# Kernel tuning notes

Measured on AMD Instinct MI355X. Metric: run time of the kernel, lower is better.

Reference implementation:

```python
import jax, jax.numpy as jnp
import numpy as np

# NTU RGB+D 25-joint skeleton edges (1-based)
NTU_EDGES = [(1,2),(2,21),(3,21),(4,3),(5,21),(6,5),(7,6),(8,7),(9,21),(10,9),
             (11,10),(12,11),(13,1),(14,13),(15,14),(16,15),(17,1),(18,17),
             (19,18),(20,19),(22,23),(23,8),(24,25),(25,12)]
NUM_SCALES = 13
NUM_POINT = 25


def build_A_powers(num_scales=NUM_SCALES, v=NUM_POINT):
    # MS-G3D disentangled multi-scale aggregation: exact-k-hop adjacencies, each
    # with self loops, symmetrically normalized, stacked along dim 0 -> (K*V, V).
    A = np.zeros((v, v))
    for i, j in NTU_EDGES:
        A[i - 1, j - 1] = 1.0
        A[j - 1, i - 1] = 1.0
    I = np.eye(v)
    mats = []
    for k in range(num_scales):
        if k == 0:
            Ak = I.copy()
        else:
            Ak = np.minimum(np.linalg.matrix_power(A + I, k), 1) \
               - np.minimum(np.linalg.matrix_power(A + I, k - 1), 1)
            Ak = Ak + I  # with_self=True
        d = Ak.sum(-1)
        dinv = np.where(d > 0, d ** -0.5, 0.0)
        mats.append((dinv[:, None] * Ak) * dinv[None, :])
    return np.concatenate(mats, 0).astype(np.float32)


def batchnorm(x, g, b, axes, ch_axis, eps=1e-5):
    # torch BatchNorm in training mode: biased batch stats + affine
    mean = jnp.mean(x, axes, keepdims=True)
    var = jnp.mean((x - mean) ** 2, axes, keepdims=True)
    shape = [1] * x.ndim
    shape[ch_axis] = -1
    return (x - mean) * jax.lax.rsqrt(var + eps) * g.reshape(shape) + b.reshape(shape)


def ms_gcn(x, A_powers, A_res, W, b, g, beta, num_scales):
    # x: (N, C, T, V); A: (K*V, V)
    A = A_powers + A_res
    support = jnp.einsum('vu,nctu->nctv', A, x)            # (N, C, T, K*V)
    N, C, T, KV = support.shape
    V = KV // num_scales
    support = support.reshape(N, C, T, num_scales, V).transpose(0, 3, 1, 2, 4)
    support = support.reshape(N, num_scales * C, T, V)     # (N, K*C, T, V)
    out = jnp.einsum('oc,nctv->notv', W, support) + b[None, :, None, None]  # 1x1 conv
    out = batchnorm(out, g, beta, (0, 2, 3), 1)
    return jax.nn.relu(out)


def lstm(x, Wih, Whh, bih, bhh):
    # single-layer batch_first LSTM, zero initial state; torch gate order i,f,g,o
    B = x.shape[0]
    H = Whh.shape[1]
    xp = jnp.einsum('bsd,hd->bsh', x, Wih) + bih + bhh     # precompute input proj

    def step(carry, xt):
        h, c = carry
        gates = xt + h @ Whh.T
        i, f, g, o = jnp.split(gates, 4, axis=-1)
        c = jax.nn.sigmoid(f) * c + jax.nn.sigmoid(i) * jnp.tanh(g)
        h = jax.nn.sigmoid(o) * jnp.tanh(c)
        return (h, c), h

    init = (jnp.zeros((B, H), x.dtype), jnp.zeros((B, H), x.dtype))
    _, ys = jax.lax.scan(step, init, jnp.swapaxes(xp, 0, 1))
    return jnp.swapaxes(ys, 0, 1)                          # (B, S, H)


def logsig_rnn(x, n_segments, Wih, Whh, bih, bhh):
    # x: (B, T, d). Depth-2 log-signature per time segment + segment start point,
    # concatenated and fed to an LSTM (Logsig-RNN layer).
    B, T, d = x.shape
    t_vec = np.array([int(round(float(v))) for v in np.linspace(1, T, n_segments + 1)])
    starts = t_vec[:-1] - 1
    ends = t_vec[1:] - 1
    L = int((ends - starts).max()) + 1
    # pad segments to fixed length by repeating the last point (zero increments)
    idx = np.minimum(starts[:, None] + np.arange(L)[None, :], ends[:, None])  # (S, L)
    pts = x[:, idx, :]                                     # (B, S, L, d)
    rel = pts - pts[:, :, :1, :]
    inc = rel[:, :, -1, :]                                 # level-1: total increment
    dx = pts[:, :, 1:, :] - pts[:, :, :-1, :]
    Mm = jnp.einsum('bsli,bslj->bsij', rel[:, :, :-1, :], dx)
    iu, ju = np.triu_indices(d, k=1)
    levy = 0.5 * (Mm[:, :, iu, ju] - Mm[:, :, ju, iu])     # level-2 (Lyndon basis)
    feats = jnp.concatenate([x[:, starts, :], inc, levy], axis=-1)
    return lstm(feats, Wih, Whh, bih, bhh)


def setup_inputs() -> dict:
    key = jax.random.key(0)
    ks = iter(jax.random.split(key, 16))
    N, C, T, V, M = 2, 3, 100, 25, 2
    c1, c2, num_class, K = 96, 192, 60, NUM_SCALES

    def randn(shape, scale):
        return jax.random.normal(next(ks), shape, jnp.float32) * scale

    ls1 = c1 + c1 * (c1 - 1) // 2     # 4656
    ls2 = c2 + c2 * (c2 - 1) // 2     # 18528
    in1 = c1 + ls1                    # 4752
    in2 = c2 + ls2                    # 18720
    Ap = jnp.asarray(build_A_powers())
    return {
        'x': jax.random.normal(next(ks), (N, C, T, V, M), jnp.float32),
        'length': jax.random.randint(next(ks), (N,), 0, T),
        'data_bn_g': jnp.ones((M * V * C,)), 'data_bn_b': jnp.zeros((M * V * C,)),
        'A_powers1': Ap,
        'A_res1': jax.random.uniform(next(ks), Ap.shape, jnp.float32, -1e-6, 1e-6),
        'W1': randn((c1, K * C), (K * C) ** -0.5), 'b1': jnp.zeros((c1,)),
        'bn1_g': jnp.ones((c1,)), 'bn1_b': jnp.zeros((c1,)),
        'Wih1': randn((4 * c1, in1), in1 ** -0.5), 'Whh1': randn((4 * c1, c1), c1 ** -0.5),
        'bih1': jnp.zeros((4 * c1,)), 'bhh1': jnp.zeros((4 * c1,)),
        'bnseg1_g': jnp.ones((50,)), 'bnseg1_b': jnp.zeros((50,)),
        'A_powers2': Ap,
        'A_res2': jax.random.uniform(next(ks), Ap.shape, jnp.float32, -1e-6, 1e-6),
        'W2': randn((c2, K * c1), (K * c1) ** -0.5), 'b2': jnp.zeros((c2,)),
        'bn2_g': jnp.ones((c2,)), 'bn2_b': jnp.zeros((c2,)),
        'Wih2': randn((4 * c2, in2), in2 ** -0.5), 'Whh2': randn((4 * c2, c2), c2 ** -0.5),
        'bih2': jnp.zeros((4 * c2,)), 'bhh2': jnp.zeros((4 * c2,)),
        'bnseg2_g': jnp.ones((30,)), 'bnseg2_b': jnp.zeros((30,)),
        'fcW': randn((num_class, c2), c2 ** -0.5), 'fcb': jnp.zeros((num_class,)),
    }


def reference(x, length, data_bn_g, data_bn_b, A_powers1, A_res1, W1, b1, bn1_g, bn1_b,
              Wih1, Whh1, bih1, bhh1, bnseg1_g, bnseg1_b, A_powers2, A_res2, W2, b2,
              bn2_g, bn2_b, Wih2, Whh2, bih2, bhh2, bnseg2_g, bnseg2_b, fcW, fcb):
    # `length` is accepted but unused, as in the original forward.
    N, C, T, V, M = x.shape
    K = A_powers1.shape[0] // V
    c1, c2 = W1.shape[0], W2.shape[0]
    S1, S2 = 50, 30

    h = x.transpose(0, 4, 3, 1, 2).reshape(N, M * V * C, T)
    h = batchnorm(h, data_bn_g, data_bn_b, (0, 2), 1)
    h = h.reshape(N * M, V, C, T).transpose(0, 2, 3, 1)            # (NM, C, T, V)

    h = jax.nn.relu(ms_gcn(h, A_powers1, A_res1, W1, b1, bn1_g, bn1_b, K))
    h = h.transpose(0, 3, 2, 1).reshape(N * M * V, T, c1)
    h = logsig_rnn(h, S1, Wih1, Whh1, bih1, bhh1)                  # (NMV, S1, c1)
    h = batchnorm(h, bnseg1_g, bnseg1_b, (0, 2), 1)
    h = h.reshape(N * M, V, S1, c1).transpose(0, 3, 2, 1)          # (NM, c1, S1, V)

    h = jax.nn.relu(ms_gcn(h, A_powers2, A_res2, W2, b2, bn2_g, bn2_b, K))
    h = h.transpose(0, 3, 2, 1).reshape(N * M * V, S1, c2)
    h = logsig_rnn(h, S2, Wih2, Whh2, bih2, bhh2)                  # (NMV, S2, c2)
    h = batchnorm(h, bnseg2_g, bnseg2_b, (0, 2), 1)
    h = h.reshape(N * M, V, S2, c2).transpose(0, 3, 2, 1)          # (NM, c2, S2, V)

    pooled = h.reshape(N, M, c2, -1).mean(axis=3).mean(axis=1)     # (N, c2)
    return pooled @ fcW.T + fcb
```

## Files before the change

kernel.cpp:

```cpp
#include <hip/hip_runtime.h>
#include <cmath>
#include <cstdint>
#include <cstddef>

typedef unsigned short bf16_t;
typedef __attribute__((ext_vector_type(8))) short short8;
typedef __attribute__((ext_vector_type(4))) float floatx4;
typedef __attribute__((ext_vector_type(2))) _Float16 half2_t;

__device__ __forceinline__ float bf2f(bf16_t b){
  unsigned int u = ((unsigned int)b) << 16;
  return __uint_as_float(u);
}
__device__ __forceinline__ bf16_t f2bf(float f){
  unsigned int u = __float_as_uint(f);
  unsigned int r = (u + 0x7fffu + ((u >> 16) & 1u)) >> 16;
  return (bf16_t)r;
}
__device__ __forceinline__ unsigned int f2bf2(float a, float b){
  return (unsigned int)f2bf(a) | ((unsigned int)f2bf(b) << 16);
}
__device__ __forceinline__ float sigf(float x){ return 1.0f / (1.0f + expf(-x)); }

__device__ __forceinline__ float dot2(half2_t a, half2_t b, float c){
#if __has_builtin(__builtin_amdgcn_fdot2)
  return __builtin_amdgcn_fdot2(a, b, c, false);
#else
  return c + (float)a.x * (float)b.x + (float)a.y * (float)b.y;
#endif
}

__device__ __forceinline__ void gload_lds16(const bf16_t* g, bf16_t* lds){
  __builtin_amdgcn_global_load_lds(
      (const __attribute__((address_space(1))) unsigned int*)g,
      (__attribute__((address_space(3))) unsigned int*)lds, 16, 0, 0);
}

__device__ __forceinline__ void barrier_raw(){
  asm volatile("s_barrier" ::: "memory");
}

__device__ __forceinline__ int xcd_chunk_swizzle(int orig, int nwg){
  int q = nwg >> 3, r = nwg & 7;
  int xcd = orig & 7, idx = orig >> 3;
  return (xcd < r ? xcd * (q + 1) : r * (q + 1) + (xcd - r) * q) + idx;
}

__global__ void prep_misc(const float* __restrict__ a1, const float* __restrict__ r1, float* __restrict__ o1,
                          const float* __restrict__ a2, const float* __restrict__ r2, float* __restrict__ o2,
                          const float* __restrict__ bi1, const float* __restrict__ bh1, float* __restrict__ ob1,
                          const float* __restrict__ bi2, const float* __restrict__ bh2, float* __restrict__ ob2,
                          const float* __restrict__ Whh1, half2_t* __restrict__ Wp1,
                          const float* __restrict__ Whh2, half2_t* __restrict__ Wp2,
                          unsigned short* __restrict__ lut1, unsigned short* __restrict__ lut2,
                          float* __restrict__ stats, bf16_t* __restrict__ A2mat){
  int i = blockIdx.x * blockDim.x + threadIdx.x;
  if (i < 8125){ o1[i] = a1[i] + r1[i]; o2[i] = a2[i] + r2[i]; }
  if (i < 384) ob1[i] = bi1[i] + bh1[i];
  if (i < 768) ob2[i] = bi2[i] + bh2[i];
  if (i < 736) stats[i] = 0.f;
  if (i < 18432){
    int t = i % 384, j2 = i / 384;
    half2_t w; w.x = (_Float16)Whh1[(size_t)t * 96 + 2 * j2];
    w.y = (_Float16)Whh1[(size_t)t * 96 + 2 * j2 + 1];
    Wp1[i] = w;
  }
  if (i < 73728){
    int t = i % 768, j2 = i / 768;
    half2_t w; w.x = (_Float16)Whh2[(size_t)t * 192 + 2 * j2];
    w.y = (_Float16)Whh2[(size_t)t * 192 + 2 * j2 + 1];
    Wp2[i] = w;
  }
  if (i < 4560){
    int d = 96, p = i;
    int r = (int)(((2.0 * d - 1.0) - sqrt((2.0 * d - 1.0) * (2.0 * d - 1.0) - 8.0 * (double)p)) * 0.5);
    if (r < 0) r = 0;
    while (r + 1 <= d - 2 && (r + 1) * (d - 1) - ((r + 1) * r) / 2 <= p) ++r;
    while (r > 0 && r * (d - 1) - (r * (r - 1)) / 2 > p) --r;
    int jj = p - (r * (d - 1) - (r * (r - 1)) / 2);
    lut1[p] = (unsigned short)((r << 8) | (r + 1 + jj));
  }
  if (i < 18336){
    int d = 192, p = i;
    int r = (int)(((2.0 * d - 1.0) - sqrt((2.0 * d - 1.0) * (2.0 * d - 1.0) - 8.0 * (double)p)) * 0.5);
    if (r < 0) r = 0;
    while (r + 1 <= d - 2 && (r + 1) * (d - 1) - ((r + 1) * r) / 2 <= p) ++r;
    while (r > 0 && r * (d - 1) - (r * (r - 1)) / 2 > p) --r;
    int jj = p - (r * (d - 1) - (r * (r - 1)) / 2);
    lut2[p] = (unsigned short)((r << 8) | (r + 1 + jj));
  }
  if (i < 160000){
    int row = i >> 5, col = 1248 + (i & 31);
    A2mat[(size_t)row * 1280 + col] = 0;
  }
}

__device__ __forceinline__ void f2bf_seg(const float* in, bf16_t* out, int Kin, int Kout, int li){
  int ko8 = Kout >> 3;
  int r = li / ko8, k8 = (li % ko8) << 3;
  uint4 u;
  if (k8 + 8 <= Kin){
    const float4* p = reinterpret_cast<const float4*>(in + (size_t)r * Kin + k8);
    float4 x0 = p[0], x1 = p[1];
    u.x = f2bf2(x0.x, x0.y); u.y = f2bf2(x0.z, x0.w);
    u.z = f2bf2(x1.x, x1.y); u.w = f2bf2(x1.z, x1.w);
  } else {
    u.x = u.y = u.z = u.w = 0u;
  }
  *reinterpret_cast<uint4*>(out + (size_t)r * Kout + k8) = u;
}

__global__ void f2bf_pad8_3(const float* __restrict__ in1, bf16_t* __restrict__ out1, int Kin1, int Kout1, int c1,
                            const float* __restrict__ in2, bf16_t* __restrict__ out2, int Kin2, int Kout2, int c2,
                            const float* __restrict__ in3, bf16_t* __restrict__ out3, int Kin3, int Kout3, int c3){
  int idx = blockIdx.x * blockDim.x + threadIdx.x;
  if (idx < c1){ f2bf_seg(in1, out1, Kin1, Kout1, idx); return; }
  idx -= c1;
  if (idx < c2){ f2bf_seg(in2, out2, Kin2, Kout2, idx); return; }
  idx -= c2;
  if (idx < c3) f2bf_seg(in3, out3, Kin3, Kout3, idx);
}

__global__ void data_bn_kernel(const float* __restrict__ x, const float* __restrict__ g,
                               const float* __restrict__ bb, float* __restrict__ h1,
                               int N, int C, int T, int V, int M){
  int ch = blockIdx.x;
  int m = ch / (V * C);
  int v = (ch / C) % V;
  int c = ch % C;
  int tid = threadIdx.x;
  int cnt = N * T;
  float s = 0.f, s2 = 0.f;
  for (int i = tid; i < cnt; i += 64){
    int n = i / T, t = i % T;
    float val = x[(((size_t)(n * C + c) * T + t) * V + v) * M + m];
    s += val; s2 += val * val;
  }
  for (int off = 32; off; off >>= 1){ s += __shfl_down(s, off); s2 += __shfl_down(s2, off); }
  s = __shfl(s, 0); s2 = __shfl(s2, 0);
  float mean = s / cnt;
  float rstd = rsqrtf(s2 / cnt - mean * mean + 1e-5f);
  float gg = g[ch], bo = bb[ch];
  for (int i = tid; i < cnt; i += 64){
    int n = i / T, t = i % T;
    float val = x[(((size_t)(n * C + c) * T + t) * V + v) * M + m];
    float y = (val - mean) * rstd * gg + bo;
    h1[((size_t)((n * M + m) * C + c) * T + t) * V + v] = y;
  }
}

__global__ __launch_bounds__(256)
void gcn1_fused(const float* __restrict__ A, const float* __restrict__ h1,
                const float* __restrict__ W1, const float* __restrict__ b1,
                float* __restrict__ y1, float* __restrict__ ssum, float* __restrict__ ssq, int T){
  __shared__ float h[3][25];
  __shared__ float sup[3][325];
  __shared__ float lsum[96], lsq[96];
  int blk = blockIdx.x;
  int nm = blk / T, t = blk % T;
  int tid = threadIdx.x;
  if (tid < 75){
    int c = tid / 25, v = tid % 25;
    h[c][v] = h1[((size_t)(nm * 3 + c) * T + t) * 25 + v];
  }
  if (tid < 96){ lsum[tid] = 0.f; lsq[tid] = 0.f; }
  __syncthreads();
  for (int w = tid; w < 975; w += 256){
    int c = w / 325, ww = w % 325;
    const float* ar = A + ww * 25;
    float acc = 0.f;
    #pragma unroll
    for (int u = 0; u < 25; ++u) acc += ar[u] * h[c][u];
    sup[c][ww] = acc;
  }
  __syncthreads();
  for (int o2 = tid; o2 < 2400; o2 += 256){
    int v = o2 / 96, o = o2 % 96;
    float acc = b1[o];
    #pragma unroll
    for (int k = 0; k < 13; ++k)
      #pragma unroll
      for (int c = 0; c < 3; ++c)
        acc += W1[o * 39 + k * 3 + c] * sup[c][k * 25 + v];
    y1[((size_t)blk * 25 + v) * 96 + o] = acc;
    atomicAdd(&lsum[o], acc);
    atomicAdd(&lsq[o], acc * acc);
  }
  __syncthreads();
  if (tid < 96){ atomicAdd(&ssum[tid], lsum[tid]); atomicAdd(&ssq[tid], lsq[tid]); }
}

struct SegTable { int st[50]; int en[50]; };

__global__ void feats_bn_kernel(const float* __restrict__ ymat, const float* __restrict__ sum,
                                const float* __restrict__ sumsq, const float* __restrict__ g,
                                const float* __restrict__ bb, bf16_t* __restrict__ feats,
                                SegTable segs, const unsigned int* __restrict__ lut32,
                                int T, int d, int S, int L, int pairs, int rowlenP, int R){
  __shared__ float pts[4][192];
  int bs = blockIdx.x;
  int b = bs / S, s = bs % S;
  int nm = b / 25, v = b % 25;
  int st = segs.st[s], en = segs.en[s];
  int nt = blockDim.x, tid = threadIdx.x;
  for (int l = 0; l < L; ++l){
    int t = st + l; if (t > en) t = en;
    const float* yrow = ymat + ((size_t)(nm * T + t) * 25 + v) * d;
    for (int i = tid; i < d; i += nt){
      float mean = sum[i] / R;
      float rstd = rsqrtf(sumsq[i] / R - mean * mean + 1e-5f);
      pts[l][i] = fmaxf((yrow[i] - mean) * rstd * g[i] + bb[i], 0.f);
    }
  }
  __syncthreads();
  unsigned int* frow32 = reinterpret_cast<unsigned int*>(feats + (size_t)bs * rowlenP);
  int d2 = d >> 1;
  for (int i2 = tid; i2 < d2; i2 += nt){
    int i = 2 * i2;
    frow32[i2]      = f2bf2(pts[0][i], pts[0][i + 1]);
    frow32[d2 + i2] = f2bf2(pts[L - 1][i] - pts[0][i], pts[L - 1][i + 1] - pts[0][i + 1]);
  }
  int rowlen2 = (2 * d + pairs) >> 1, rowlenP2 = rowlenP >> 1;
  for (int i = tid + rowlen2; i < rowlenP2; i += nt) frow32[i] = 0;
  int Lm2 = L - 2;
  unsigned int* lrow32 = frow32 + d;
  int pairs2 = pairs >> 1;
  for (int p2 = tid; p2 < pairs2; p2 += nt){
    unsigned int ee = lut32[p2];
    int i0 = (ee >> 8) & 255, j0 = ee & 255;
    int i1 = ee >> 24, j1 = (ee >> 16) & 255;
    float acc0 = 0.f, acc1 = 0.f;
    for (int l = 1; l <= Lm2; ++l){
      float ri = pts[l][i0] - pts[0][i0], rj = pts[l][j0] - pts[0][j0];
      float di = pts[l + 1][i0] - pts[l][i0], dj = pts[l + 1][j0] - pts[l][j0];
      acc0 += ri * dj - rj * di;
      float ri1 = pts[l][i1] - pts[0][i1], rj1 = pts[l][j1] - pts[0][j1];
      float di1 = pts[l + 1][i1] - pts[l][i1], dj1 = pts[l + 1][j1] - pts[l][j1];
      acc1 += ri1 * dj1 - rj1 * di1;
    }
    lrow32[p2] = f2bf2(0.5f * acc0, 0.5f * acc1);
  }
}

__global__ __launch_bounds__(256)
void gemm_mfma_nt_split(const bf16_t* __restrict__ A, const bf16_t* __restrict__ B,
                        float* __restrict__ P, int M, int N, int K,
                        int GX, int GY, int GZ){
  __shared__ bf16_t As[128 * 64];
  __shared__ bf16_t Bs[128 * 64];
  const int nwg = GX * GY * GZ;
  const int wg = xcd_chunk_swizzle(blockIdx.x, nwg);
  const int bxi = wg % GX, byi = (wg / GX) % GY, bzi = wg / (GX * GY);
  const int tid = threadIdx.x;
  const int lane = tid & 63, wv = tid >> 6;
  const int bm = bxi * 128, bn = byi * 128;
  const int wr = (wv >> 1) * 64, wc = (wv & 1) * 64;
  const int m_l = lane & 15, q = lane >> 4;

  const int ksteps = K >> 6;
  const int Z = GZ, z = bzi;
  const int per = (ksteps + Z - 1) / Z;
  const int ks0 = z * per;
  const int ks1 = (ks0 + per < ksteps) ? ks0 + per : ksteps;

  const int rlane = lane >> 3;
  const int slane = lane & 7;
  const int colc = (slane ^ rlane) * 8;
  const bf16_t* gA[4]; const bf16_t* gB[4];
  bf16_t* lA[4]; bf16_t* lB[4];
  #pragma unroll
  for (int it = 0; it < 4; ++it){
    int c = it * 4 + wv;
    int rowA = bm + c * 8 + rlane; if (rowA > M - 1) rowA = M - 1;
    int rowB = bn + c * 8 + rlane; if (rowB > N - 1) rowB = N - 1;
    gA[it] = A + (size_t)rowA * K + colc;
    gB[it] = B + (size_t)rowB * K + colc;
    lA[it] = &As[c * 512];
    lB[it] = &Bs[c * 512];
  }
  const int sxor = m_l & 7;

  floatx4 acc[4][4] = {};
  for (int ks = ks0; ks < ks1; ++ks){
    int k0 = ks << 6;
    __syncthreads();
    #pragma unroll
    for (int it = 0; it < 4; ++it){
      gload_lds16(gA[it] + k0, lA[it]);
      gload_lds16(gB[it] + k0, lB[it]);
    }
    __syncthreads();
    #pragma unroll
    for (int half = 0; half < 2; ++half){
      const int scol = ((half * 4 + q) ^ sxor) * 8;
      short8 af[4], bfr[4];
      #pragma unroll
      for (int i = 0; i < 4; ++i){
        af[i]  = *reinterpret_cast<const short8*>(&As[(wr + i * 16 + m_l) * 64 + scol]);
        bfr[i] = *reinterpret_cast<const short8*>(&Bs[(wc + i * 16 + m_l) * 64 + scol]);
      }
      #pragma unroll
      for (int mi = 0; mi < 4; ++mi)
        #pragma unroll
        for (int ni = 0; ni < 4; ++ni)
          acc[mi][ni] = __builtin_amdgcn_mfma_f32_16x16x32_bf16(af[mi], bfr[ni], acc[mi][ni], 0, 0, 0);
    }
  }

  float* Pz = P + (size_t)z * M * N;
  #pragma unroll
  for (int mi = 0; mi < 4; ++mi){
    int row0 = bm + wr + mi * 16 + q * 4;
    #pragma unroll
    for (int r = 0; r < 4; ++r){
      int row = row0 + r;
      if (row < M){
        #pragma unroll
        for (int ni = 0; ni < 4; ++ni){
          int col = bn + wc + ni * 16 + m_l;
          if (col < N) Pz[(size_t)row * N + col] = acc[mi][ni][r];
        }
      }
    }
  }
}

#define VMC4 asm volatile("s_waitcnt vmcnt(4)" ::: "memory")
#define VMC0 asm volatile("s_waitcnt vmcnt(0)" ::: "memory")
#define STG_A8(NB, KH, OFF) { gload_lds16(pA0 + (OFF) + (KH) * 32, dA0 + (NB) * 16384 + (KH) * 8192); \
                              gload_lds16(pA1 + (OFF) + (KH) * 32, dA1 + (NB) * 16384 + (KH) * 8192); }
#define STG_B8(NB, KH, OFF) { gload_lds16(pB0 + (OFF) + (KH) * 32, dB0 + (NB) * 16384 + (KH) * 8192); \
                              gload_lds16(pB1 + (OFF) + (KH) * 32, dB1 + (NB) * 16384 + (KH) * 8192); }
#define PH8(BUF, KH, MIB, LOADB, STAGE_BLOCK, WAIT_BLOCK) { \
    const bf16_t* ab_ = As + (BUF) * 16384 + (KH) * 8192 + sA + (MIB) * 512; \
    _Pragma("unroll") \
    for (int i_ = 0; i_ < 4; ++i_) af[i_] = *reinterpret_cast<const short8*>(ab_ + i_ * 512); \
    if (LOADB){ \
      const bf16_t* bb_ = Bs + (BUF) * 16384 + (KH) * 8192 + sB; \
      _Pragma("unroll") \
      for (int i_ = 0; i_ < 4; ++i_) bfr[i_] = *reinterpret_cast<const short8*>(bb_ + i_ * 512); \
    } \
    STAGE_BLOCK; \
    WAIT_BLOCK; \
    barrier_raw(); \
    __builtin_amdgcn_s_setprio(1); \
    _Pragma("unroll") \
    for (int mi_ = 0; mi_ < 4; ++mi_) \
      _Pragma("unroll") \
      for (int ni_ = 0; ni_ < 4; ++ni_) \
        acc[(MIB) + mi_][ni_] = __builtin_amdgcn_mfma_f32_16x16x32_bf16(af[mi_], bfr[ni_], acc[(MIB) + mi_][ni_], 0, 0, 0); \
    __builtin_amdgcn_s_setprio(0); \
    barrier_raw(); \
  }

__global__ __launch_bounds__(512, 2)
void gemm_mfma_nt_8ph(const bf16_t* __restrict__ A, const bf16_t* __restrict__ B,
                      float* __restrict__ P, int M, int N, int K,
                      int GX, int GY, int GZ){
  __shared__ bf16_t As[32768];
  __shared__ bf16_t Bs[32768];
  const int nwg = GX * GY * GZ;
  const int wg = xcd_chunk_swizzle(blockIdx.x, nwg);
  const int bxi = wg % GX, byi = (wg / GX) % GY, bzi = wg / (GX * GY);
  const int tid = threadIdx.x;
  const int lane = tid & 63, wv = tid >> 6;
  const int wm = wv >> 2, wn = wv & 3;
  const int m_l = lane & 15, q = lane >> 4;
  const int bm = bxi * 256, bn = byi * 256;

  const int ksteps = K >> 6;
  const int z = bzi, Z = GZ;
  const int per = (ksteps + Z - 1) / Z;
  const int ks0 = z * per;
  int ks1 = ks0 + per; if (ks1 > ksteps) ks1 = ksteps;
  if (ks0 >= ks1) return;

  const int rlane = lane >> 2, slane = lane & 3;
  const int cg = slane ^ ((rlane >> 1) & 3);
  int rr0 = wv * 16 + rlane, rr1 = (8 + wv) * 16 + rlane;
  int ra0 = bm + rr0; if (ra0 > M - 1) ra0 = M - 1;
  int ra1 = bm + rr1; if (ra1 > M - 1) ra1 = M - 1;
  int rb0 = bn + rr0; if (rb0 > N - 1) rb0 = N - 1;
  int rb1 = bn + rr1; if (rb1 > N - 1) rb1 = N - 1;
  const bf16_t* pA0 = A + (size_t)ra0 * K + cg * 8 + ks0 * 64;
  const bf16_t* pA1 = A + (size_t)ra1 * K + cg * 8 + ks0 * 64;
  const bf16_t* pB0 = B + (size_t)rb0 * K + cg * 8 + ks0 * 64;
  const bf16_t* pB1 = B + (size_t)rb1 * K + cg * 8 + ks0 * 64;
  bf16_t* dA0 = As + wv * 512;
  bf16_t* dA1 = As + (8 + wv) * 512;
  bf16_t* dB0 = Bs + wv * 512;
  bf16_t* dB1 = Bs + (8 + wv) * 512;

  const int sA = (wm * 128 + m_l) * 32 + ((q ^ ((m_l >> 1) & 3)) * 8);
  const int sB = (wn * 64 + m_l) * 32 + ((q ^ ((m_l >> 1) & 3)) * 8);

  short8 af[4], bfr[4];
  floatx4 acc[8][4] = {};

  STG_A8(0, 0, 0); STG_B8(0, 0, 0); STG_A8(0, 1, 0); STG_B8(0, 1, 0);
  VMC4;
  barrier_raw();

  int buf = 0;
  for (int t = ks0; t < ks1 - 1; ++t){
    const int nb = buf ^ 1;
    PH8(buf, 0, 0, true,  STG_A8(nb, 0, 64), ((void)0));
    PH8(buf, 0, 4, false, STG_B8(nb, 0, 64), VMC4);
    PH8(buf, 1, 0, true,  STG_A8(nb, 1, 64), ((void)0));
    PH8(buf, 1, 4, false, STG_B8(nb, 1, 64), VMC4);
    pA0 += 64; pA1 += 64; pB0 += 64; pB1 += 64;
    buf = nb;
  }
  PH8(buf, 0, 0, true,  ((void)0), ((void)0));
  PH8(buf, 0, 4, false, ((void)0), VMC0);
  PH8(buf, 1, 0, true,  ((void)0), ((void)0));
  PH8(buf, 1, 4, false, ((void)0), ((void)0));

  float* Pz = P + (size_t)z * M * N;
  #pragma unroll
  for (int mi = 0; mi < 8; ++mi){
    int row0 = bm + wm * 128 + mi * 16 + q * 4;
    #pragma unroll
    for (int r = 0; r < 4; ++r){
      int row = row0 + r;
      if (row < M){
        #pragma unroll
        for (int ni = 0; ni < 4; ++ni){
          int col = bn + wn * 64 + ni * 16 + m_l;
          if (col < N) Pz[(size_t)row * N + col] = acc[mi][ni][r];
        }
      }
    }
  }
}

__global__ __launch_bounds__(256)
void reduce_split_bias_stats(const float* __restrict__ P, const float* __restrict__ bias,
                             float* __restrict__ out, float* __restrict__ ssum, float* __restrict__ ssq,
                             int MN, int N, int Z){
  __shared__ float lsum[192], lsq[192];
  int tid = threadIdx.x;
  if (tid < 192){ lsum[tid] = 0.f; lsq[tid] = 0.f; }
  __syncthreads();
  int i4 = (blockIdx.x * blockDim.x + tid) * 4;
  if (i4 < MN){
    const float4 bv = *reinterpret_cast<const float4*>(bias + (i4 % N));
    float4 s = bv;
    for (int z = 0; z < Z; ++z){
      const float4 p = *reinterpret_cast<const float4*>(P + (size_t)z * MN + i4);
      s.x += p.x; s.y += p.y; s.z += p.z; s.w += p.w;
    }
    *reinterpret_cast<float4*>(out + i4) = s;
    int c0 = i4 % N;
    atomicAdd(&lsum[c0],     s.x); atomicAdd(&lsq[c0],     s.x * s.x);
    atomicAdd(&lsum[c0 + 1], s.y); atomicAdd(&lsq[c0 + 1], s.y * s.y);
    atomicAdd(&lsum[c0 + 2], s.z); atomicAdd(&lsq[c0 + 2], s.z * s.z);
    atomicAdd(&lsum[c0 + 3], s.w); atomicAdd(&lsq[c0 + 3], s.w * s.w);
  }
  __syncthreads();
  if (tid < 192){ atomicAdd(&ssum[tid], lsum[tid]); atomicAdd(&ssq[tid], lsq[tid]); }
}

template <int H2C, int BLK, int Z>
__global__ __launch_bounds__(BLK)
void lstm_kernel(const float* __restrict__ P, const float* __restrict__ bias,
                 const half2_t* __restrict__ Wp, float* __restrict__ out,
                 float* __restrict__ ssum, float* __restrict__ ssq,
                 int S, int MN){
  constexpr int H = 2 * H2C;
  constexpr int H4 = 4 * H;
  __shared__ _Float16 __attribute__((aligned(16))) hsh[H];
  __shared__ float gv[H4];
  __shared__ float ra[BLK / 64], rb[BLK / 64];
  const int b = blockIdx.x, t = threadIdx.x;
  const int lane = t & 63, wid = t >> 6;
  half2_t w[H2C];
  const half2_t* wp = Wp + t;
  #pragma unroll
  for (int j2 = 0; j2 < H2C; ++j2) w[j2] = wp[(size_t)j2 * H4];
  float cc = 0.f;
  if (t < H) hsh[t] = (_Float16)0.f;
  const float bval = bias[t];
  const size_t base = (size_t)b * S * H4 + t;
  float pv0[Z], pv1[Z];
  #pragma unroll
  for (int z = 0; z < Z; ++z) pv0[z] = P[(size_t)z * MN + base];
  #pragma unroll
  for (int z = 0; z < Z; ++z) pv1[z] = P[(size_t)z * MN + base + H4];
  __syncthreads();
  const half2_t* hp = reinterpret_cast<const half2_t*>(hsh);
  for (int s = 0; s < S; ++s){
    float pvn[Z];
    if (s + 2 < S){
      size_t o2 = base + (size_t)(s + 2) * H4;
      #pragma unroll
      for (int z = 0; z < Z; ++z) pvn[z] = P[(size_t)z * MN + o2];
    }
    float a0 = bval, a1 = 0.f, a2 = 0.f, a3 = 0.f;
    float a4 = 0.f, a5 = 0.f, a6 = 0.f, a7 = 0.f;
    #pragma unroll
    for (int z = 0; z < Z; ++z) a0 += pv0[z];
    #pragma unroll
    for (int j2 = 0; j2 < H2C; j2 += 8){
      a0 = dot2(w[j2],     hp[j2],     a0);
      a1 = dot2(w[j2 + 1], hp[j2 + 1], a1);
      a2 = dot2(w[j2 + 2], hp[j2 + 2], a2);
      a3 = dot2(w[j2 + 3], hp[j2 + 3], a3);
      a4 = dot2(w[j2 + 4], hp[j2 + 4], a4);
      a5 = dot2(w[j2 + 5], hp[j2 + 5], a5);
      a6 = dot2(w[j2 + 6], hp[j2 + 6], a6);
      a7 = dot2(w[j2 + 7], hp[j2 + 7], a7);
    }
    gv[t] = ((a0 + a1) + (a2 + a3)) + ((a4 + a5) + (a6 + a7));
    __syncthreads();
    float gvv = 0.f;
    if (t < H){
      float ig = sigf(gv[t]);
      float fg = sigf(gv[H + t]);
      float gg = tanhf(gv[2 * H + t]);
      float og = sigf(gv[3 * H + t]);
      cc = fg * cc + ig * gg;
      float hh = og * tanhf(cc);
      hsh[t] = (_Float16)hh;
      out[((size_t)b * S + s) * H + t] = hh;
      gvv = hh;
    }
    float q1 = gvv, q2 = gvv * gvv;
    for (int off2 = 32; off2; off2 >>= 1){ q1 += __shfl_down(q1, off2); q2 += __shfl_down(q2, off2); }
    if (lane == 0){ ra[wid] = q1; rb[wid] = q2; }
    __syncthreads();
    if (t == 0){
      float sa = 0.f, sb = 0.f;
      #pragma unroll
      for (int ww = 0; ww < BLK / 64; ++ww){ sa += ra[ww]; sb += rb[ww]; }
      atomicAdd(&ssum[s], sa);
      atomicAdd(&ssq[s], sb);
    }
    #pragma unroll
    for (int z = 0; z < Z; ++z){ pv0[z] = pv1[z]; pv1[z] = pvn[z]; }
  }
}

__global__ void support2_bn(const float* __restrict__ A, const float* __restrict__ lout,
                            const float* __restrict__ ssum, const float* __restrict__ ssq,
                            const float* __restrict__ g, const float* __restrict__ bb,
                            bf16_t* __restrict__ A2mat, int S, int cnt){
  int idx = blockIdx.x * blockDim.x + threadIdx.x;
  int total = 4 * S * 25 * 13 * 96;
  if (idx >= total) return;
  int c = idx % 96;
  int k = (idx / 96) % 13;
  int v = (idx / (96 * 13)) % 25;
  int rs = idx / (96 * 13 * 25);
  int s = rs % S, nm = rs / S;
  float mean = ssum[s] / cnt;
  float rstd = rsqrtf(ssq[s] / cnt - mean * mean + 1e-5f);
  float scale = rstd * g[s];
  float shift = bb[s] - mean * scale;
  const float* ar = A + (k * 25 + v) * 25;
  float acc = 0.f;
  #pragma unroll
  for (int u = 0; u < 25; ++u){
    float raw = lout[((size_t)(nm * 25 + u) * S + s) * 96 + c];
    acc += ar[u] * (raw * scale + shift);
  }
  A2mat[((size_t)rs * 25 + v) * 1280 + k * 96 + c] = f2bf(acc);
}

__global__ void pool_kernel(const float* __restrict__ lout2, const float* __restrict__ sum,
                            const float* __restrict__ sumsq, const float* __restrict__ g,
                            const float* __restrict__ bb, float* __restrict__ pooled,
                            int S, int H, int scnt){
  int n = blockIdx.x / H;
  int o = blockIdx.x % H;
  float acc = 0.f;
  int cnt = 2 * 25 * S;
  for (int i = threadIdx.x; i < cnt; i += 64){
    int m = i / (25 * S);
    int r = i % (25 * S);
    int v = r / S;
    int s = r % S;
    int b = (n * 2 + m) * 25 + v;
    float val = lout2[((size_t)b * S + s) * H + o];
    float mean = sum[s] / scnt;
    float rstd = rsqrtf(sumsq[s] / scnt - mean * mean + 1e-5f);
    val = (val - mean) * rstd * g[s] + bb[s];
    acc += val;
  }
  for (int off = 32; off; off >>= 1) acc += __shfl_down(acc, off);
  if (threadIdx.x == 0) pooled[n * H + o] = acc / cnt;
}

__global__ void fc_kernel(const float* __restrict__ pooled, const float* __restrict__ fcW,
                          const float* __restrict__ fcb, float* __restrict__ outp){
  int idx = blockIdx.x * blockDim.x + threadIdx.x;
  if (idx >= 120) return;
  int n = idx / 60, cls = idx % 60;
  float acc = fcb[cls];
  for (int o = 0; o < 192; ++o) acc += pooled[n * 192 + o] * fcW[cls * 192 + o];
  outp[idx] = acc;
}

static void make_segs(int T, int S, SegTable& tab, int& L){
  double step = (double)(T - 1) / (double)S;
  long long tv[51];
  for (int i = 0; i <= S; ++i){
    double v = 1.0 + step * (double)i;
    tv[i] = llrint(v);
  }
  L = 0;
  for (int s = 0; s < S; ++s){
    tab.st[s] = (int)tv[s] - 1;
    tab.en[s] = (int)tv[s + 1] - 1;
    int len = tab.en[s] - tab.st[s] + 1;
    if (len > L) L = len;
  }
  for (int s = S; s < 50; ++s){ tab.st[s] = 0; tab.en[s] = 0; }
  if (L > 4) L = 4;
}

extern "C" void kernel_launch(void* const* d_in, const int* in_sizes, int n_in,
                              void* d_out, int out_size, void* d_ws, size_t ws_size,
                              hipStream_t stream){
  const float* x         = (const float*)d_in[0];
  const float* data_bn_g = (const float*)d_in[2];
  const float* data_bn_b = (const float*)d_in[3];
  const float* A_powers1 = (const float*)d_in[4];
  const float* A_res1    = (const float*)d_in[5];
  const float* W1        = (const float*)d_in[6];
  const float* b1        = (const float*)d_in[7];
  const float* bn1_g     = (const float*)d_in[8];
  const float* bn1_b     = (const float*)d_in[9];
  const float* Wih1      = (const float*)d_in[10];
  const float* Whh1      = (const float*)d_in[11];
  const float* bih1      = (const float*)d_in[12];
  const float* bhh1      = (const float*)d_in[13];
  const float* bnseg1_g  = (const float*)d_in[14];
  const float* bnseg1_b  = (const float*)d_in[15];
  const float* A_powers2 = (const float*)d_in[16];
  const float* A_res2    = (const float*)d_in[17];
  const float* W2        = (const float*)d_in[18];
  const float* b2        = (const float*)d_in[19];
  const float* bn2_g     = (const float*)d_in[20];
  const float* bn2_b     = (const float*)d_in[21];
  const float* Wih2      = (const float*)d_in[22];
  const float* Whh2      = (const float*)d_in[23];
  const float* bih2      = (const float*)d_in[24];
  const float* bhh2      = (const float*)d_in[25];
  const float* bnseg2_g  = (const float*)d_in[26];
  const float* bnseg2_b  = (const float*)d_in[27];
  const float* fcW       = (const float*)d_in[28];
  const float* fcb       = (const float*)d_in[29];
  float* out = (float*)d_out;

  const int N = 2, C = 3, T = 100, V = 25, M = 2, NM = 4;
  const int C1 = 96, C2 = 192;
  const int S1 = 50, S2 = 30;
  const int B = 100;
  const int IN1 = 4752, IN2 = 18720;
  const int IN1P = 4800, IN2P = 18752;
  const int P1 = 4560, P2 = 18336;
  const int KG2 = 1248, KG2P = 1280;
  const int Z1 = 5, Z2 = 7, ZG = 4;

  size_t off = 0;
  char* base = (char*)d_ws;
  auto alloc = [&](size_t nbytes) -> void* {
    off = (off + 255) & ~(size_t)255;
    void* p = base + off;
    off += nbytes;
    return p;
  };
  float* A1full = (float*)alloc(325 * 25 * 4);
  float* A2full = (float*)alloc(325 * 25 * 4);
  float* h1     = (float*)alloc((size_t)NM * C * T * V * 4);
  float* y1mat  = (float*)alloc((size_t)NM * T * V * C1 * 4);
  float* stats  = (float*)alloc(736 * 4);
  float* st1a = stats, *st1b = stats + 96;
  float* sg1a = stats + 192, *sg1b = stats + 242;
  float* st2a = stats + 292, *st2b = stats + 484;
  float* sg2a = stats + 676, *sg2b = stats + 706;
  float* l1out  = (float*)alloc((size_t)B * S1 * C1 * 4);
  bf16_t* A2mat = (bf16_t*)alloc((size_t)NM * S1 * V * KG2P * 2);
  float* y2mat  = (float*)alloc((size_t)NM * S1 * V * C2 * 4);
  float* l2out  = (float*)alloc((size_t)B * S2 * C2 * 4);
  float* pooled = (float*)alloc(2 * C2 * 4);
  float* bias1  = (float*)alloc(4 * C1 * 4);
  float* bias2  = (float*)alloc(4 * C2 * 4);
  half2_t* Wp1  = (half2_t*)alloc((size_t)(C1 / 2) * 4 * C1 * 4);
  half2_t* Wp2  = (half2_t*)alloc((size_t)(C2 / 2) * 4 * C2 * 4);
  bf16_t* Wih1b = (bf16_t*)alloc((size_t)4 * C1 * IN1P * 2);
  bf16_t* Wih2b = (bf16_t*)alloc((size_t)4 * C2 * IN2P * 2);
  bf16_t* W2b   = (bf16_t*)alloc((size_t)C2 * KG2P * 2);
  unsigned short* lut1 = (unsigned short*)alloc((size_t)P1 * 2);
  unsigned short* lut2 = (unsigned short*)alloc((size_t)P2 * 2);
  size_t pmax = (size_t)Z2 * 3000 * 768;
  {
    size_t p1s = (size_t)Z1 * 5000 * 384; if (p1s > pmax) pmax = p1s;
    size_t pgs = (size_t)ZG * 5000 * 192; if (pgs > pmax) pmax = pgs;
  }
  float* Pbuf = (float*)alloc(pmax * 4);
  bf16_t* feats = (bf16_t*)alloc((size_t)B * S2 * IN2P * 2);
  (void)ws_size; (void)in_sizes; (void)n_in; (void)out_size;

  prep_misc<<<625, 256, 0, stream>>>(A_powers1, A_res1, A1full, A_powers2, A_res2, A2full,
                                     bih1, bhh1, bias1, bih2, bhh2, bias2,
                                     Whh1, Wp1, Whh2, Wp2, lut1, lut2, stats, A2mat);
  {
    int c1 = 4 * C1 * (IN1P / 8);
    int c2 = 4 * C2 * (IN2P / 8);
    int c3 = C2 * (KG2P / 8);
    int tot = c1 + c2 + c3;
    f2bf_pad8_3<<<(tot + 255) / 256, 256, 0, stream>>>(Wih1, Wih1b, IN1, IN1P, c1,
                                                       Wih2, Wih2b, IN2, IN2P, c2,
                                                       W2, W2b, KG2, KG2P, c3);
  }

  data_bn_kernel<<<M * V * C, 64, 0, stream>>>(x, data_bn_g, data_bn_b, h1, N, C, T, V, M);

  gcn1_fused<<<NM * T, 256, 0, stream>>>(A1full, h1, W1, b1, y1mat, st1a, st1b, T);

  SegTable seg1, seg2; int L1, L2;
  make_segs(T, S1, seg1, L1);
  make_segs(S1, S2, seg2, L2);

  feats_bn_kernel<<<B * S1, 256, 0, stream>>>(y1mat, st1a, st1b, bn1_g, bn1_b, feats, seg1,
                                              (const unsigned int*)lut1, T, C1, S1, L1, P1, IN1P,
                                              NM * T * 25);
  {
    int Mm = B * S1, Nn = 4 * C1;
    int GX = (Mm + 127) / 128, GY = (Nn + 127) / 128;
    gemm_mfma_nt_split<<<GX * GY * Z1, 256, 0, stream>>>(feats, Wih1b, Pbuf, Mm, Nn, IN1P,
                                                         GX, GY, Z1);
    lstm_kernel<48, 384, Z1><<<B, 384, 0, stream>>>(Pbuf, bias1, Wp1, l1out, sg1a, sg1b, S1, Mm * Nn);
  }

  {
    int tot = NM * S1 * 25 * 13 * 96;
    support2_bn<<<(tot + 255) / 256, 256, 0, stream>>>(A2full, l1out, sg1a, sg1b, bnseg1_g,
                                                       bnseg1_b, A2mat, S1, B * C1);
  }
  {
    int Mm = NM * S1 * 25, Nn = C2;
    int GX = (Mm + 127) / 128, GY = (Nn + 127) / 128;
    gemm_mfma_nt_split<<<GX * GY * ZG, 256, 0, stream>>>(A2mat, W2b, Pbuf, Mm, Nn, KG2P,
                                                         GX, GY, ZG);
    int MN = Mm * Nn;
    reduce_split_bias_stats<<<(MN / 4 + 255) / 256, 256, 0, stream>>>(Pbuf, b2, y2mat, st2a, st2b,
                                                                      MN, Nn, ZG);
  }

  feats_bn_kernel<<<B * S2, 256, 0, stream>>>(y2mat, st2a, st2b, bn2_g, bn2_b, feats, seg2,
                                              (const unsigned int*)lut2, S1, C2, S2, L2, P2, IN2P,
                                              NM * S1 * 25);
  {
    int Mm = B * S2, Nn = 4 * C2;
    int GX = (Mm + 255) / 256, GY = (Nn + 255) / 256;
    gemm_mfma_nt_8ph<<<GX * GY * Z2, 512, 0, stream>>>(feats, Wih2b, Pbuf, Mm, Nn, IN2P,
                                                       GX, GY, Z2);
    lstm_kernel<96, 768, Z2><<<B, 768, 0, stream>>>(Pbuf, bias2, Wp2, l2out, sg2a, sg2b, S2, Mm * Nn);
  }

  pool_kernel<<<2 * C2, 64, 0, stream>>>(l2out, sg2a, sg2b, bnseg2_g, bnseg2_b, pooled, S2, C2, B * C2);
  fc_kernel<<<1, 128, 0, stream>>>(pooled, fcW, fcb, out);
}
```

Before: 666.3 us.

## Double-buffer LDS fragment registers to overlap reads with MFMA in GEMM

Restructures the 8-phase bf16 MFMA GEMM main loop so each phase issues LDS reads for the next phase's A/B fragments while the current phase's MFMAs run. It uses ping-pong register sets and prefetches the next k-step's first fragments at the end of each iteration. The goal is to hide LDS read latency behind matrix-core work, since the old loop read fragments and then waited before computing. The cost is higher VGPR pressure from the doubled fragment registers at 2 waves/SIMD occupancy, plus a more delicate barrier/ordering scheme where a race or spill could appear.

```diff
diff --git a/kernel.cpp b/kernel.cpp
--- a/kernel.cpp
+++ b/kernel.cpp
@@ -331,27 +331,29 @@
                               gload_lds16(pA1 + (OFF) + (KH) * 32, dA1 + (NB) * 16384 + (KH) * 8192); }
 #define STG_B8(NB, KH, OFF) { gload_lds16(pB0 + (OFF) + (KH) * 32, dB0 + (NB) * 16384 + (KH) * 8192); \
                               gload_lds16(pB1 + (OFF) + (KH) * 32, dB1 + (NB) * 16384 + (KH) * 8192); }
-#define PH8(BUF, KH, MIB, LOADB, STAGE_BLOCK, WAIT_BLOCK) { \
-    const bf16_t* ab_ = As + (BUF) * 16384 + (KH) * 8192 + sA + (MIB) * 512; \
+#define READ_AF(DST, BUF, KH, MIB) { \
+    const bf16_t* pr_ = As + (BUF) * 16384 + (KH) * 8192 + sA + (MIB) * 512; \
     _Pragma("unroll") \
-    for (int i_ = 0; i_ < 4; ++i_) af[i_] = *reinterpret_cast<const short8*>(ab_ + i_ * 512); \
-    if (LOADB){ \
-      const bf16_t* bb_ = Bs + (BUF) * 16384 + (KH) * 8192 + sB; \
-      _Pragma("unroll") \
-      for (int i_ = 0; i_ < 4; ++i_) bfr[i_] = *reinterpret_cast<const short8*>(bb_ + i_ * 512); \
-    } \
-    STAGE_BLOCK; \
-    WAIT_BLOCK; \
-    barrier_raw(); \
-    __builtin_amdgcn_s_setprio(1); \
+    for (int i_ = 0; i_ < 4; ++i_) DST[i_] = *reinterpret_cast<const short8*>(pr_ + i_ * 512); }
+#define READ_BF(DST, BUF, KH) { \
+    const bf16_t* pr_ = Bs + (BUF) * 16384 + (KH) * 8192 + sB; \
+    _Pragma("unroll") \
+    for (int i_ = 0; i_ < 4; ++i_) DST[i_] = *reinterpret_cast<const short8*>(pr_ + i_ * 512); }
+#define MFMA_BLK(AF, BF, MIB) \
     _Pragma("unroll") \
     for (int mi_ = 0; mi_ < 4; ++mi_) \
       _Pragma("unroll") \
       for (int ni_ = 0; ni_ < 4; ++ni_) \
-        acc[(MIB) + mi_][ni_] = __builtin_amdgcn_mfma_f32_16x16x32_bf16(af[mi_], bfr[ni_], acc[(MIB) + mi_][ni_], 0, 0, 0); \
+        acc[(MIB) + mi_][ni_] = __builtin_amdgcn_mfma_f32_16x16x32_bf16(AF[mi_], BF[ni_], acc[(MIB) + mi_][ni_], 0, 0, 0);
+#define PIPE_PH(STAGE_BLOCK, WAIT_BLOCK, READS_BLOCK, AF, BF, MIB) { \
+    STAGE_BLOCK; \
+    WAIT_BLOCK; \
+    barrier_raw(); \
+    READS_BLOCK; \
+    __builtin_amdgcn_s_setprio(1); \
+    MFMA_BLK(AF, BF, MIB); \
     __builtin_amdgcn_s_setprio(0); \
-    barrier_raw(); \
-  }
+    barrier_raw(); }
 
 __global__ __launch_bounds__(512, 2)
 void gemm_mfma_nt_8ph(const bf16_t* __restrict__ A, const bf16_t* __restrict__ B,
@@ -394,27 +396,40 @@
   const int sA = (wm * 128 + m_l) * 32 + ((q ^ ((m_l >> 1) & 3)) * 8);
   const int sB = (wn * 64 + m_l) * 32 + ((q ^ ((m_l >> 1) & 3)) * 8);
 
-  short8 af[4], bfr[4];
+  short8 afA[4], afB[4], bfA[4], bfB[4];
   floatx4 acc[8][4] = {};
 
   STG_A8(0, 0, 0); STG_B8(0, 0, 0); STG_A8(0, 1, 0); STG_B8(0, 1, 0);
   VMC4;
   barrier_raw();
+  READ_AF(afA, 0, 0, 0);
+  READ_BF(bfA, 0, 0);
 
   int buf = 0;
   for (int t = ks0; t < ks1 - 1; ++t){
     const int nb = buf ^ 1;
-    PH8(buf, 0, 0, true,  STG_A8(nb, 0, 64), ((void)0));
-    PH8(buf, 0, 4, false, STG_B8(nb, 0, 64), VMC4);
-    PH8(buf, 1, 0, true,  STG_A8(nb, 1, 64), ((void)0));
-    PH8(buf, 1, 4, false, STG_B8(nb, 1, 64), VMC4);
+    PIPE_PH(STG_A8(nb, 0, 64), ((void)0),
+            { READ_AF(afB, buf, 0, 4); }, afA, bfA, 0);
+    PIPE_PH(STG_B8(nb, 0, 64), VMC4,
+            { READ_AF(afA, buf, 1, 0); READ_BF(bfB, buf, 1); }, afB, bfA, 4);
+    PIPE_PH(STG_A8(nb, 1, 64), ((void)0),
+            { READ_AF(afB, buf, 1, 4); }, afA, bfB, 0);
+    PIPE_PH(STG_B8(nb, 1, 64), VMC4,
+            { READ_AF(afA, nb, 0, 0); READ_BF(bfA, nb, 0); }, afB, bfB, 4);
     pA0 += 64; pA1 += 64; pB0 += 64; pB1 += 64;
     buf = nb;
   }
-  PH8(buf, 0, 0, true,  ((void)0), ((void)0));
-  PH8(buf, 0, 4, false, ((void)0), VMC0);
-  PH8(buf, 1, 0, true,  ((void)0), ((void)0));
-  PH8(buf, 1, 4, false, ((void)0), ((void)0));
+  READ_AF(afB, buf, 0, 4);
+  __builtin_amdgcn_s_setprio(1); MFMA_BLK(afA, bfA, 0); __builtin_amdgcn_s_setprio(0);
+  VMC0;
+  barrier_raw();
+  READ_AF(afA, buf, 1, 0); READ_BF(bfB, buf, 1);
+  __builtin_amdgcn_s_setprio(1); MFMA_BLK(afB, bfA, 4); __builtin_amdgcn_s_setprio(0);
+  READ_AF(afB, buf, 1, 4);
+  __builtin_amdgcn_s_setprio(1);
+  MFMA_BLK(afA, bfB, 0);
+  MFMA_BLK(afB, bfB, 4);
+  __builtin_amdgcn_s_setprio(0);
 
   float* Pz = P + (size_t)z * M * N;
   #pragma unroll
```

Result: no change. 667.5 us (+0.2%).
